# Performance work log

Hardware: AMD Instinct MI355X
Metric: run time of the kernel (lower is better)

The kernel has to match this reference:

```python
import jax, jax.numpy as jnp
import numpy as np

N = 50000
E = 800000
IN_DIM = 128
HIDDEN = 32
HEADS = 4
OUT_DIM = 64
NEG_SLOPE = 0.2


def _glorot(key, shape):
    fan_in, fan_out = shape[0], shape[-1]
    lim = jnp.sqrt(6.0 / (fan_in + fan_out))
    return jax.random.uniform(key, shape, jnp.float32, -lim, lim)


def setup_inputs() -> dict:
    key = jax.random.key(0)
    ks = jax.random.split(key, 16)
    x = jax.random.normal(ks[0], (N, IN_DIM), jnp.float32)
    edge_index = jax.random.randint(ks[1], (2, E), 0, N, jnp.int64)
    # layer 0: in_dim -> hidden, heads, concat
    W1 = _glorot(ks[2], (IN_DIM, HEADS * HIDDEN))
    a_src1 = _glorot(ks[3], (HEADS, HIDDEN))
    a_dst1 = _glorot(ks[4], (HEADS, HIDDEN))
    b1 = jnp.zeros((HEADS * HIDDEN,), jnp.float32)
    # layer 1: hidden*heads -> hidden, heads, concat
    W2 = _glorot(ks[5], (HEADS * HIDDEN, HEADS * HIDDEN))
    a_src2 = _glorot(ks[6], (HEADS, HIDDEN))
    a_dst2 = _glorot(ks[7], (HEADS, HIDDEN))
    b2 = jnp.zeros((HEADS * HIDDEN,), jnp.float32)
    # layer 2: hidden*heads -> out_dim, heads, concat=False (mean over heads)
    W3 = _glorot(ks[8], (HEADS * HIDDEN, HEADS * OUT_DIM))
    a_src3 = _glorot(ks[9], (HEADS, OUT_DIM))
    a_dst3 = _glorot(ks[10], (HEADS, OUT_DIM))
    b3 = jnp.zeros((OUT_DIM,), jnp.float32)
    return {"x": x, "edge_index": edge_index,
            "W1": W1, "a_src1": a_src1, "a_dst1": a_dst1, "b1": b1,
            "W2": W2, "a_src2": a_src2, "a_dst2": a_dst2, "b2": b2,
            "W3": W3, "a_src3": a_src3, "a_dst3": a_dst3, "b3": b3}


def gat_conv(x, src, dst, W, a_src, a_dst, bias, out_ch, concat):
    # linear projection, per-head view: [N, H, C]
    h = (x @ W).reshape(N, HEADS, out_ch)
    # per-node attention logits, gathered to edges: [E, H]
    alpha_src = jnp.einsum('nhc,hc->nh', h, a_src)
    alpha_dst = jnp.einsum('nhc,hc->nh', h, a_dst)
    e = jax.nn.leaky_relu(alpha_src[src] + alpha_dst[dst], NEG_SLOPE)
    # segment softmax over incoming edges of each dst node
    m = jax.ops.segment_max(e, dst, num_segments=N)  # [N, H]
    m = jnp.where(jnp.isfinite(m), m, 0.0)
    p = jnp.exp(e - m[dst])  # [E, H]
    denom = jax.ops.segment_sum(p, dst, num_segments=N)  # [N, H]
    alpha = p / (denom[dst] + 1e-16)
    # weighted scatter-add of source features: [N, H, C]
    out = jax.ops.segment_sum(h[src] * alpha[:, :, None], dst, num_segments=N)
    if concat:
        return out.reshape(N, HEADS * out_ch) + bias
    return out.mean(axis=1) + bias


def reference(x, edge_index, W1, a_src1, a_dst1, b1, W2, a_src2, a_dst2, b2,
              W3, a_src3, a_dst3, b3):
    src, dst = edge_index[0], edge_index[1]
    x = gat_conv(x, src, dst, W1, a_src1, a_dst1, b1, HIDDEN, True)
    x = gat_conv(x, src, dst, W2, a_src2, a_dst2, b2, HIDDEN, True)
    x = gat_conv(x, src, dst, W3, a_src3, a_dst3, b3, OUT_DIM, False)
    return x
```

## Files before the change

kernel.cpp:

```cpp
#include <hip/hip_runtime.h>
#include <hip/hip_fp16.h>
#include <math.h>

#define NNODES 50000
#define NEDGES 800000

typedef _Float16 half8 __attribute__((ext_vector_type(8)));
typedef float floatx4 __attribute__((ext_vector_type(4)));


__global__ void zero_i32(int* __restrict__ p, int n) {
    int i = blockIdx.x * 256 + threadIdx.x;
    if (i < n) p[i] = 0;
}

__global__ void hist_kernel(const int* __restrict__ dst, int* __restrict__ counts, int e) {
    int i = blockIdx.x * 256 + threadIdx.x;
    if (i < e) atomicAdd(&counts[dst[i]], 1);
}

__global__ void scan1_kernel(const int* __restrict__ counts, int* __restrict__ row_ptr,
                             int* __restrict__ bsums, int n) {
    __shared__ int s[256];
    int tid = threadIdx.x;
    int i = blockIdx.x * 256 + tid;
    int v = (i < n) ? counts[i] : 0;
    s[tid] = v;
    __syncthreads();
    #pragma unroll
    for (int o = 1; o < 256; o <<= 1) {
        int t = (tid >= o) ? s[tid - o] : 0;
        __syncthreads();
        s[tid] += t;
        __syncthreads();
    }
    if (i < n) row_ptr[i + 1] = s[tid];
    if (tid == 255) bsums[blockIdx.x] = s[255];
}

__global__ void scan2_kernel(int* __restrict__ bsums, int nb) {
    __shared__ int s[256];
    int tid = threadIdx.x;
    int v = (tid < nb) ? bsums[tid] : 0;
    s[tid] = v;
    __syncthreads();
    #pragma unroll
    for (int o = 1; o < 256; o <<= 1) {
        int t = (tid >= o) ? s[tid - o] : 0;
        __syncthreads();
        s[tid] += t;
        __syncthreads();
    }
    if (tid < nb) bsums[tid] = s[tid] - v;
}

__global__ void scan3_kernel(int* __restrict__ row_ptr, const int* __restrict__ bsums, int n) {
    int i = blockIdx.x * 256 + threadIdx.x;
    if (i < n) row_ptr[i + 1] += bsums[blockIdx.x];
    if (i == 0) row_ptr[0] = 0;
}

__global__ void fill_kernel(const int* __restrict__ src, const int* __restrict__ dst,
                            const int* __restrict__ row_ptr, int* __restrict__ cursor,
                            int* __restrict__ csr_src, int e) {
    int i = blockIdx.x * 256 + threadIdx.x;
    if (i < e) {
        int d = dst[i];
        int pos = atomicAdd(&cursor[d], 1);
        csr_src[row_ptr[d] + pos] = src[i];
    }
}


__global__ void convert_x(const float* __restrict__ x, __half* __restrict__ xh, int total4) {
    int i = blockIdx.x * 256 + threadIdx.x;
    if (i < total4) {
        float4 v = *(const float4*)&x[i * 4];
        __half2 a = __floats2half2_rn(v.x, v.y);
        __half2 b = __floats2half2_rn(v.z, v.w);
        uint2 st = {*(unsigned int*)&a, *(unsigned int*)&b};
        *(uint2*)&xh[i * 4] = st;
    }
}

__global__ void convert_wt(const float* __restrict__ W, __half* __restrict__ Wt, int M) {
    int i = blockIdx.x * 256 + threadIdx.x;
    if (i < 128 * M) {
        int k = i / M, nn = i - k * M;
        Wt[nn * 128 + k] = __float2half(W[i]);
    }
}


template <int CH>
__global__ __launch_bounds__(256, 3) void gemm_mfma(const __half* __restrict__ A,
                                                    const __half* __restrict__ Wt,
                                                    const float* __restrict__ a_src,
                                                    const float* __restrict__ a_dst,
                                                    __half* __restrict__ H,
                                                    float* __restrict__ asrc,
                                                    float* __restrict__ adst, int n, int M) {
    __shared__ __half As[128][136];
    __shared__ __half Ws[64][136];
    __shared__ float scr[2][128][2];
    int tid = threadIdx.x;
    int row0 = blockIdx.x * 128;
    int col0 = blockIdx.y * 64;

    #pragma unroll
    for (int it = 0; it < 8; ++it) {
        int flat = tid + it * 256;
        int r = flat >> 4;
        int kq = (flat & 15) * 8;
        int gr = row0 + r;
        float4 v = {0.f, 0.f, 0.f, 0.f};
        if (gr < n) v = *(const float4*)&A[(size_t)gr * 128 + kq];
        *(float4*)&As[r][kq] = v;
    }
    #pragma unroll
    for (int it = 0; it < 4; ++it) {
        int flat = tid + it * 256;
        int r = flat >> 4;
        int kq = (flat & 15) * 8;
        *(float4*)&Ws[r][kq] = *(const float4*)&Wt[(size_t)(col0 + r) * 128 + kq];
    }
    __syncthreads();

    int lane = tid & 63;
    int wid = tid >> 6;
    int wm = (wid >> 1) * 64;
    int wn = (wid & 1) * 32;
    int l15 = lane & 15;
    int l4 = lane >> 4;

    floatx4 acc[4][2];
    #pragma unroll
    for (int mf = 0; mf < 4; ++mf)
        #pragma unroll
        for (int nf = 0; nf < 2; ++nf) {
            floatx4 z = {0.f, 0.f, 0.f, 0.f};
            acc[mf][nf] = z;
        }

    #pragma unroll
    for (int ks = 0; ks < 4; ++ks) {
        int kb = ks * 32 + l4 * 8;
        half8 b0 = *(const half8*)&Ws[wn + l15][kb];
        half8 b1 = *(const half8*)&Ws[wn + 16 + l15][kb];
        #pragma unroll
        for (int mf = 0; mf < 4; ++mf) {
            half8 a = *(const half8*)&As[wm + mf * 16 + l15][kb];
            acc[mf][0] = __builtin_amdgcn_mfma_f32_16x16x32_f16(a, b0, acc[mf][0], 0, 0, 0);
            acc[mf][1] = __builtin_amdgcn_mfma_f32_16x16x32_f16(a, b1, acc[mf][1], 0, 0, 0);
        }
    }

    #pragma unroll
    for (int mf = 0; mf < 4; ++mf)
        #pragma unroll
        for (int r = 0; r < 4; ++r) {
            int gr = row0 + wm + mf * 16 + l4 * 4 + r;
            if (gr < n) {
                H[(size_t)gr * M + col0 + wn + l15] = __float2half(acc[mf][0][r]);
                H[(size_t)gr * M + col0 + wn + 16 + l15] = __float2half(acc[mf][1][r]);
            }
        }

    int hw = (col0 + wn) / CH;
    int cb = (col0 + wn) % CH;
    float vs0 = a_src[hw * CH + cb + l15];
    float vs1 = a_src[hw * CH + cb + 16 + l15];
    float vd0 = a_dst[hw * CH + cb + l15];
    float vd1 = a_dst[hw * CH + cb + 16 + l15];

    #pragma unroll
    for (int mf = 0; mf < 4; ++mf)
        #pragma unroll
        for (int r = 0; r < 4; ++r) {
            float ss = acc[mf][0][r] * vs0 + acc[mf][1][r] * vs1;
            float sd = acc[mf][0][r] * vd0 + acc[mf][1][r] * vd1;
            #pragma unroll
            for (int o = 1; o < 16; o <<= 1) {
                ss += __shfl_xor(ss, o);
                sd += __shfl_xor(sd, o);
            }
            if (l15 == 0) {
                int ri = wm + mf * 16 + l4 * 4 + r;
                if constexpr (CH == 32) {
                    int gr = row0 + ri;
                    if (gr < n) {
                        asrc[(size_t)gr * 4 + hw] = ss;
                        adst[(size_t)gr * 4 + hw] = sd;
                    }
                } else {
                    scr[wid & 1][ri][0] = ss;
                    scr[wid & 1][ri][1] = sd;
                }
            }
        }
    if constexpr (CH == 64) {
        __syncthreads();
        if (tid < 128) {
            int gr = row0 + tid;
            if (gr < n) {
                int head = col0 / 64;
                asrc[(size_t)gr * 4 + head] = scr[0][tid][0] + scr[1][tid][0];
                adst[(size_t)gr * 4 + head] = scr[0][tid][1] + scr[1][tid][1];
            }
        }
    }
}


template <int CPL, bool MEAN>
__global__ __launch_bounds__(256) void aggregate_kernel(
    const __half* __restrict__ h, const float* __restrict__ asrc,
    const float* __restrict__ adst, const int* __restrict__ csr_src,
    const int* __restrict__ row_ptr, const float* __restrict__ bias,
    void* __restrict__ out_, int n) {
    __shared__ float lds[4][332];
    int wid = threadIdx.x >> 6;
    int lane = threadIdx.x & 63;
    int node = blockIdx.x * 4 + wid;
    if (node >= n) return;
    float* Wp = lds[wid];
    int* Ws = (int*)&lds[wid][264];
    int start = row_ptr[node];
    int end = row_ptr[node + 1];
    float4 ad = *(const float4*)&adst[(size_t)node * 4];

    int l32, head, j_off;
    if constexpr (CPL == 2) {
        l32 = lane & 31; head = l32 >> 3; j_off = lane >> 5;
    } else {
        l32 = lane; head = lane >> 4; j_off = 0;
    }
    int hoff = head * 66;

    float acc0 = 0.f, acc1 = 0.f, acc2 = 0.f, acc3 = 0.f, pw = 0.f;

    for (int base = start; base < end; base += 64) {
        int cnt = end - base;
        if (cnt > 64) cnt = 64;
        int s = 0;
        float4 pv = {0.f, 0.f, 0.f, 0.f};
        if (lane < cnt) {
            s = csr_src[base + lane];
            float4 a = *(const float4*)&asrc[(size_t)s * 4];
            float e0 = a.x + ad.x; e0 = (e0 > 0.f) ? e0 : 0.2f * e0;
            float e1 = a.y + ad.y; e1 = (e1 > 0.f) ? e1 : 0.2f * e1;
            float e2 = a.z + ad.z; e2 = (e2 > 0.f) ? e2 : 0.2f * e2;
            float e3 = a.w + ad.w; e3 = (e3 > 0.f) ? e3 : 0.2f * e3;
            pv.x = __expf(e0); pv.y = __expf(e1); pv.z = __expf(e2); pv.w = __expf(e3);
        }
        Wp[0 * 66 + lane] = pv.x;
        Wp[1 * 66 + lane] = pv.y;
        Wp[2 * 66 + lane] = pv.z;
        Wp[3 * 66 + lane] = pv.w;
        Ws[lane] = s;
        __builtin_amdgcn_wave_barrier();
        asm volatile("" ::: "memory");
        if constexpr (CPL == 2) {
            #pragma unroll 4
            for (int jj = 0; jj < cnt; jj += 2) {
                int j = jj + j_off;
                float w = Wp[hoff + j];
                int s2 = Ws[j];
                float2 raw = *(const float2*)(h + (size_t)s2 * 128 + l32 * 4);
                __half2 p01 = ((const __half2*)&raw)[0];
                __half2 p23 = ((const __half2*)&raw)[1];
                float2 f01 = __half22float2(p01);
                float2 f23 = __half22float2(p23);
                acc0 += w * f01.x;
                acc1 += w * f01.y;
                acc2 += w * f23.x;
                acc3 += w * f23.y;
                pw += w;
            }
        } else {
            #pragma unroll 4
            for (int j = 0; j < cnt; ++j) {
                float w = Wp[hoff + j];
                int s2 = Ws[j];
                float2 raw = *(const float2*)(h + (size_t)s2 * 256 + lane * 4);
                __half2 p01 = ((const __half2*)&raw)[0];
                __half2 p23 = ((const __half2*)&raw)[1];
                float2 f01 = __half22float2(p01);
                float2 f23 = __half22float2(p23);
                acc0 += w * f01.x;
                acc1 += w * f01.y;
                acc2 += w * f23.x;
                acc3 += w * f23.y;
                pw += w;
            }
        }
        __builtin_amdgcn_wave_barrier();
        asm volatile("" ::: "memory");
    }

    if constexpr (!MEAN) {
        acc0 += __shfl_xor(acc0, 32);
        acc1 += __shfl_xor(acc1, 32);
        acc2 += __shfl_xor(acc2, 32);
        acc3 += __shfl_xor(acc3, 32);
        pw += __shfl_xor(pw, 32);
        if (lane < 32) {
            float inv = 1.f / (pw + 1e-16f);
            float4 b = *(const float4*)&bias[l32 * 4];
            __half* out = (__half*)out_;
            __half2 ha = __floats2half2_rn(acc0 * inv + b.x, acc1 * inv + b.y);
            __half2 hb = __floats2half2_rn(acc2 * inv + b.z, acc3 * inv + b.w);
            uint2 st = {*(unsigned int*)&ha, *(unsigned int*)&hb};
            *(uint2*)&out[(size_t)node * 128 + l32 * 4] = st;
        }
    } else {
        float inv = 1.f / (pw + 1e-16f);
        float r0 = acc0 * inv, r1 = acc1 * inv, r2 = acc2 * inv, r3 = acc3 * inv;
        r0 += __shfl_xor(r0, 16); r0 += __shfl_xor(r0, 32);
        r1 += __shfl_xor(r1, 16); r1 += __shfl_xor(r1, 32);
        r2 += __shfl_xor(r2, 16); r2 += __shfl_xor(r2, 32);
        r3 += __shfl_xor(r3, 16); r3 += __shfl_xor(r3, 32);
        if (lane < 16) {
            float* out = (float*)out_;
            float4 b = *(const float4*)&bias[lane * 4];
            float4 o;
            o.x = 0.25f * r0 + b.x;
            o.y = 0.25f * r1 + b.y;
            o.z = 0.25f * r2 + b.z;
            o.w = 0.25f * r3 + b.w;
            *(float4*)&out[(size_t)node * 64 + lane * 4] = o;
        }
    }
}


extern "C" void kernel_launch(void* const* d_in, const int* in_sizes, int n_in,
                              void* d_out, int out_size, void* d_ws, size_t ws_size,
                              hipStream_t stream) {
    const float* x = (const float*)d_in[0];
    const int* ei = (const int*)d_in[1];
    const int* src = ei;
    const int* dst = ei + NEDGES;
    const float* W1 = (const float*)d_in[2];
    const float* as1 = (const float*)d_in[3];
    const float* ad1 = (const float*)d_in[4];
    const float* b1 = (const float*)d_in[5];
    const float* W2 = (const float*)d_in[6];
    const float* as2 = (const float*)d_in[7];
    const float* ad2 = (const float*)d_in[8];
    const float* b2 = (const float*)d_in[9];
    const float* W3 = (const float*)d_in[10];
    const float* as3 = (const float*)d_in[11];
    const float* ad3 = (const float*)d_in[12];
    const float* b3 = (const float*)d_in[13];

    char* ws = (char*)d_ws;
    size_t off = 0;
    auto take = [&](size_t bytes) -> char* {
        char* p = ws + off;
        off = (off + bytes + 255) & ~(size_t)255;
        return p;
    };
    int* csr = (int*)take((size_t)NEDGES * 4);
    int* row_ptr = (int*)take((size_t)(NNODES + 1) * 4);
    int* counts = (int*)take((size_t)NNODES * 4);
    int* cursor = (int*)take((size_t)NNODES * 4);
    int* bsums = (int*)take(1024 * 4);
    float* asrc = (float*)take((size_t)NNODES * 4 * 4);
    float* adst = (float*)take((size_t)NNODES * 4 * 4);
    __half* hbuf = (__half*)take((size_t)NNODES * 256 * 2);
    __half* xh = (__half*)take((size_t)NNODES * 128 * 2);
    __half* buf1h = (__half*)take((size_t)NNODES * 128 * 2);
    __half* wt = (__half*)take((size_t)256 * 128 * 2);
    float* outp = (float*)d_out;

    int nbN = (NNODES + 255) / 256;
    int nbE = (NEDGES + 255) / 256;
    int gnodeAgg = (NNODES + 3) / 4;

    zero_i32<<<nbN, 256, 0, stream>>>(counts, NNODES);
    hist_kernel<<<nbE, 256, 0, stream>>>(dst, counts, NEDGES);
    scan1_kernel<<<nbN, 256, 0, stream>>>(counts, row_ptr, bsums, NNODES);
    scan2_kernel<<<1, 256, 0, stream>>>(bsums, nbN);
    scan3_kernel<<<nbN, 256, 0, stream>>>(row_ptr, bsums, NNODES);
    zero_i32<<<nbN, 256, 0, stream>>>(cursor, NNODES);
    fill_kernel<<<nbE, 256, 0, stream>>>(src, dst, row_ptr, cursor, csr, NEDGES);

    convert_x<<<(NNODES * 128 / 4 + 255) / 256, 256, 0, stream>>>(x, xh, NNODES * 128 / 4);

    dim3 gA((NNODES + 127) / 128, 2);
    dim3 gB((NNODES + 127) / 128, 4);

    convert_wt<<<(128 * 128 + 255) / 256, 256, 0, stream>>>(W1, wt, 128);
    gemm_mfma<32><<<gA, 256, 0, stream>>>(xh, wt, as1, ad1, hbuf, asrc, adst, NNODES, 128);
    aggregate_kernel<2, false><<<gnodeAgg, 256, 0, stream>>>(hbuf, asrc, adst, csr, row_ptr, b1, buf1h, NNODES);

    convert_wt<<<(128 * 128 + 255) / 256, 256, 0, stream>>>(W2, wt, 128);
    gemm_mfma<32><<<gA, 256, 0, stream>>>(buf1h, wt, as2, ad2, hbuf, asrc, adst, NNODES, 128);
    aggregate_kernel<2, false><<<gnodeAgg, 256, 0, stream>>>(hbuf, asrc, adst, csr, row_ptr, b2, buf1h, NNODES);

    convert_wt<<<(128 * 256 + 255) / 256, 256, 0, stream>>>(W3, wt, 256);
    gemm_mfma<64><<<gB, 256, 0, stream>>>(buf1h, wt, as3, ad3, hbuf, asrc, adst, NNODES, 256);
    aggregate_kernel<4, true><<<gnodeAgg, 256, 0, stream>>>(hbuf, asrc, adst, csr, row_ptr, b3, outp, NNODES);
}
```

Baseline: 304.1 us.

## Fuse fp32-to-fp16 input and weight conversion into GEMM loads, drop extra launches

Removes the convert_x and three convert_wt kernels. The GEMM now reads fp32 x directly for layer 1 and reads fp32 weights directly, converting and transposing them into shared memory as it loads. The cursor zeroing is folded into scan3, and the CH=64 scratch buffer now reuses the As shared memory, guarded by an extra barrier. This cuts kernel launches and the intermediate xh write and read, at the cost of strided scalar transposed LDS stores for the weights in every block and more global reads of fp32 x.

```diff
diff --git a/kernel.cpp b/kernel.cpp
--- a/kernel.cpp
+++ b/kernel.cpp
@@ -54,9 +54,13 @@
     if (tid < nb) bsums[tid] = s[tid] - v;
 }
 
-__global__ void scan3_kernel(int* __restrict__ row_ptr, const int* __restrict__ bsums, int n) {
+__global__ void scan3_kernel(int* __restrict__ row_ptr, const int* __restrict__ bsums,
+                             int* __restrict__ cursor, int n) {
     int i = blockIdx.x * 256 + threadIdx.x;
-    if (i < n) row_ptr[i + 1] += bsums[blockIdx.x];
+    if (i < n) {
+        row_ptr[i + 1] += bsums[blockIdx.x];
+        cursor[i] = 0;
+    }
     if (i == 0) row_ptr[0] = 0;
 }
 
@@ -72,29 +76,9 @@
 }
 
 
-__global__ void convert_x(const float* __restrict__ x, __half* __restrict__ xh, int total4) {
-    int i = blockIdx.x * 256 + threadIdx.x;
-    if (i < total4) {
-        float4 v = *(const float4*)&x[i * 4];
-        __half2 a = __floats2half2_rn(v.x, v.y);
-        __half2 b = __floats2half2_rn(v.z, v.w);
-        uint2 st = {*(unsigned int*)&a, *(unsigned int*)&b};
-        *(uint2*)&xh[i * 4] = st;
-    }
-}
-
-__global__ void convert_wt(const float* __restrict__ W, __half* __restrict__ Wt, int M) {
-    int i = blockIdx.x * 256 + threadIdx.x;
-    if (i < 128 * M) {
-        int k = i / M, nn = i - k * M;
-        Wt[nn * 128 + k] = __float2half(W[i]);
-    }
-}
-
-
-template <int CH>
-__global__ __launch_bounds__(256, 3) void gemm_mfma(const __half* __restrict__ A,
-                                                    const __half* __restrict__ Wt,
+template <int CH, bool AF32, int LAYER>
+__global__ __launch_bounds__(256, 3) void gemm_mfma(const void* __restrict__ A_,
+                                                    const float* __restrict__ Wf,
                                                     const float* __restrict__ a_src,
                                                     const float* __restrict__ a_dst,
                                                     __half* __restrict__ H,
@@ -102,27 +86,54 @@
                                                     float* __restrict__ adst, int n, int M) {
     __shared__ __half As[128][136];
     __shared__ __half Ws[64][136];
-    __shared__ float scr[2][128][2];
+    float* scrf = (float*)&As[0][0];
     int tid = threadIdx.x;
     int row0 = blockIdx.x * 128;
     int col0 = blockIdx.y * 64;
 
+    if constexpr (AF32) {
+        const float* Af = (const float*)A_;
+        #pragma unroll
+        for (int it = 0; it < 8; ++it) {
+            int flat = tid + it * 256;
+            int r = flat >> 4;
+            int kq = (flat & 15) * 8;
+            int gr = row0 + r;
+            float4 v0 = {0.f, 0.f, 0.f, 0.f}, v1 = {0.f, 0.f, 0.f, 0.f};
+            if (gr < n) {
+                v0 = *(const float4*)&Af[(size_t)gr * 128 + kq];
+                v1 = *(const float4*)&Af[(size_t)gr * 128 + kq + 4];
+            }
+            __half2 h0 = __floats2half2_rn(v0.x, v0.y);
+            __half2 h1 = __floats2half2_rn(v0.z, v0.w);
+            __half2 h2 = __floats2half2_rn(v1.x, v1.y);
+            __half2 h3 = __floats2half2_rn(v1.z, v1.w);
+            uint4 st = {*(unsigned*)&h0, *(unsigned*)&h1, *(unsigned*)&h2, *(unsigned*)&h3};
+            *(uint4*)&As[r][kq] = st;
+        }
+    } else {
+        const __half* Ah = (const __half*)A_;
+        #pragma unroll
+        for (int it = 0; it < 8; ++it) {
+            int flat = tid + it * 256;
+            int r = flat >> 4;
+            int kq = (flat & 15) * 8;
+            int gr = row0 + r;
+            float4 v = {0.f, 0.f, 0.f, 0.f};
+            if (gr < n) v = *(const float4*)&Ah[(size_t)gr * 128 + kq];
+            *(float4*)&As[r][kq] = v;
+        }
+    }
     #pragma unroll
     for (int it = 0; it < 8; ++it) {
         int flat = tid + it * 256;
-        int r = flat >> 4;
-        int kq = (flat & 15) * 8;
-        int gr = row0 + r;
-        float4 v = {0.f, 0.f, 0.f, 0.f};
-        if (gr < n) v = *(const float4*)&A[(size_t)gr * 128 + kq];
-        *(float4*)&As[r][kq] = v;
-    }
-    #pragma unroll
-    for (int it = 0; it < 4; ++it) {
-        int flat = tid + it * 256;
-        int r = flat >> 4;
-        int kq = (flat & 15) * 8;
-        *(float4*)&Ws[r][kq] = *(const float4*)&Wt[(size_t)(col0 + r) * 128 + kq];
+        int k = flat >> 4;
+        int q = flat & 15;
+        float4 v = *(const float4*)&Wf[(size_t)k * M + col0 + q * 4];
+        Ws[q * 4 + 0][k] = __float2half(v.x);
+        Ws[q * 4 + 1][k] = __float2half(v.y);
+        Ws[q * 4 + 2][k] = __float2half(v.z);
+        Ws[q * 4 + 3][k] = __float2half(v.w);
     }
     __syncthreads();
 
@@ -154,6 +165,7 @@
             acc[mf][1] = __builtin_amdgcn_mfma_f32_16x16x32_f16(a, b1, acc[mf][1], 0, 0, 0);
         }
     }
+    if constexpr (CH == 64) __syncthreads();
 
     #pragma unroll
     for (int mf = 0; mf < 4; ++mf)
@@ -193,8 +205,8 @@
                         adst[(size_t)gr * 4 + hw] = sd;
                     }
                 } else {
-                    scr[wid & 1][ri][0] = ss;
-                    scr[wid & 1][ri][1] = sd;
+                    scrf[((wid & 1) * 128 + ri) * 2 + 0] = ss;
+                    scrf[((wid & 1) * 128 + ri) * 2 + 1] = sd;
                 }
             }
         }
@@ -204,15 +216,15 @@
             int gr = row0 + tid;
             if (gr < n) {
                 int head = col0 / 64;
-                asrc[(size_t)gr * 4 + head] = scr[0][tid][0] + scr[1][tid][0];
-                adst[(size_t)gr * 4 + head] = scr[0][tid][1] + scr[1][tid][1];
-            }
-        }
-    }
-}
-
-
-template <int CPL, bool MEAN>
+                asrc[(size_t)gr * 4 + head] = scrf[tid * 2 + 0] + scrf[(128 + tid) * 2 + 0];
+                adst[(size_t)gr * 4 + head] = scrf[tid * 2 + 1] + scrf[(128 + tid) * 2 + 1];
+            }
+        }
+    }
+}
+
+
+template <int CPL, bool MEAN, int LAYER>
 __global__ __launch_bounds__(256) void aggregate_kernel(
     const __half* __restrict__ h, const float* __restrict__ asrc,
     const float* __restrict__ adst, const int* __restrict__ csr_src,
@@ -369,9 +381,7 @@
     float* asrc = (float*)take((size_t)NNODES * 4 * 4);
     float* adst = (float*)take((size_t)NNODES * 4 * 4);
     __half* hbuf = (__half*)take((size_t)NNODES * 256 * 2);
-    __half* xh = (__half*)take((size_t)NNODES * 128 * 2);
     __half* buf1h = (__half*)take((size_t)NNODES * 128 * 2);
-    __half* wt = (__half*)take((size_t)256 * 128 * 2);
     float* outp = (float*)d_out;
 
     int nbN = (NNODES + 255) / 256;
@@ -382,24 +392,18 @@
     hist_kernel<<<nbE, 256, 0, stream>>>(dst, counts, NEDGES);
     scan1_kernel<<<nbN, 256, 0, stream>>>(counts, row_ptr, bsums, NNODES);
     scan2_kernel<<<1, 256, 0, stream>>>(bsums, nbN);
-    scan3_kernel<<<nbN, 256, 0, stream>>>(row_ptr, bsums, NNODES);
-    zero_i32<<<nbN, 256, 0, stream>>>(cursor, NNODES);
+    scan3_kernel<<<nbN, 256, 0, stream>>>(row_ptr, bsums, cursor, NNODES);
     fill_kernel<<<nbE, 256, 0, stream>>>(src, dst, row_ptr, cursor, csr, NEDGES);
-
-    convert_x<<<(NNODES * 128 / 4 + 255) / 256, 256, 0, stream>>>(x, xh, NNODES * 128 / 4);
 
     dim3 gA((NNODES + 127) / 128, 2);
     dim3 gB((NNODES + 127) / 128, 4);
 
-    convert_wt<<<(128 * 128 + 255) / 256, 256, 0, stream>>>(W1, wt, 128);
-    gemm_mfma<32><<<gA, 256, 0, stream>>>(xh, wt, as1, ad1, hbuf, asrc, adst, NNODES, 128);
-    aggregate_kernel<2, false><<<gnodeAgg, 256, 0, stream>>>(hbuf, asrc, adst, csr, row_ptr, b1, buf1h, NNODES);
-
-    convert_wt<<<(128 * 128 + 255) / 256, 256, 0, stream>>>(W2, wt, 128);
-    gemm_mfma<32><<<gA, 256, 0, stream>>>(buf1h, wt, as2, ad2, hbuf, asrc, adst, NNODES, 128);
-    aggregate_kernel<2, false><<<gnodeAgg, 256, 0, stream>>>(hbuf, asrc, adst, csr, row_ptr, b2, buf1h, NNODES);
-
-    convert_wt<<<(128 * 256 + 255) / 256, 256, 0, stream>>>(W3, wt, 256);
-    gemm_mfma<64><<<gB, 256, 0, stream>>>(buf1h, wt, as3, ad3, hbuf, asrc, adst, NNODES, 256);
-    aggregate_kernel<4, true><<<gnodeAgg, 256, 0, stream>>>(hbuf, asrc, adst, csr, row_ptr, b3, outp, NNODES);
-}
+    gemm_mfma<32, true, 1><<<gA, 256, 0, stream>>>(x, W1, as1, ad1, hbuf, asrc, adst, NNODES, 128);
+    aggregate_kernel<2, false, 1><<<gnodeAgg, 256, 0, stream>>>(hbuf, asrc, adst, csr, row_ptr, b1, buf1h, NNODES);
+
+    gemm_mfma<32, false, 2><<<gA, 256, 0, stream>>>(buf1h, W2, as2, ad2, hbuf, asrc, adst, NNODES, 128);
+    aggregate_kernel<2, false, 2><<<gnodeAgg, 256, 0, stream>>>(hbuf, asrc, adst, csr, row_ptr, b2, buf1h, NNODES);
+
+    gemm_mfma<64, false, 3><<<gB, 256, 0, stream>>>(buf1h, W3, as3, ad3, hbuf, asrc, adst, NNODES, 256);
+    aggregate_kernel<4, true, 3><<<gnodeAgg, 256, 0, stream>>>(hbuf, asrc, adst, csr, row_ptr, b3, outp, NNODES);
+}
```

Measured after the change: 295.8 us. -2.8%, faster.
